# Performance work log

Measured on AMD Instinct MI355X. Metric: run time of the kernel, lower is better.

The kernel has to match this reference:

```python
import jax, jax.numpy as jnp
import numpy as np

D_MODEL = 1024
NUM_HEADS = 16
D_K = D_MODEL // NUM_HEADS
THETA = 10000.0


def setup_inputs() -> dict:
    key = jax.random.key(0)
    ks = jax.random.split(key, 5)
    b, s = 4, 1024
    std = 1.0 / np.sqrt(D_MODEL)
    x = jax.random.normal(ks[0], (b, s, D_MODEL), dtype=jnp.float32)
    token_positions = jnp.tile(jnp.arange(s, dtype=jnp.int64)[None, :], (b, 1))
    Wq = jax.random.truncated_normal(ks[1], -3.0, 3.0, (D_MODEL, D_MODEL), jnp.float32) * std
    Wk = jax.random.truncated_normal(ks[2], -3.0, 3.0, (D_MODEL, D_MODEL), jnp.float32) * std
    Wv = jax.random.truncated_normal(ks[3], -3.0, 3.0, (D_MODEL, D_MODEL), jnp.float32) * std
    Wo = jax.random.truncated_normal(ks[4], -3.0, 3.0, (D_MODEL, D_MODEL), jnp.float32) * std
    return {"x": x, "token_positions": token_positions,
            "Wq": Wq, "Wk": Wk, "Wv": Wv, "Wo": Wo}


def _apply_rope(x):
    # x: [b, h, s, d_k]; source uses row index i (ignores token_positions)
    s, d = x.shape[-2], x.shape[-1]
    pos = jnp.arange(s, dtype=jnp.float32)                      # [s]
    kidx = jnp.arange(0, d, 2, dtype=jnp.float32)               # [d/2]
    ang = pos[:, None] / (THETA ** (kidx / d))                  # [s, d/2]
    cos, sin = jnp.cos(ang), jnp.sin(ang)
    x_even, x_odd = x[..., 0::2], x[..., 1::2]                  # [b,h,s,d/2]
    out_even = x_even * cos - x_odd * sin
    out_odd = x_even * sin + x_odd * cos
    return jnp.stack([out_even, out_odd], axis=-1).reshape(x.shape)


def reference(x, token_positions, Wq, Wk, Wv, Wo):
    b, s, _ = x.shape
    # Linear: einsum '... din, dout din -> ... dout'  => x @ W.T
    q = jnp.einsum('bsd,ed->bse', x, Wq)
    k = jnp.einsum('bsd,ed->bse', x, Wk)
    v = jnp.einsum('bsd,ed->bse', x, Wv)
    # split heads -> [b, h, s, d_k]
    def split(t):
        return t.reshape(b, s, NUM_HEADS, D_K).transpose(0, 2, 1, 3)
    q, k, v = split(q), split(k), split(v)
    q = _apply_rope(q)
    k = _apply_rope(k)
    scores = jnp.einsum('bhqd,bhkd->bhqk', q, k) / np.sqrt(D_K)
    causal = jnp.tril(jnp.ones((s, s), dtype=bool))
    scores = jnp.where(causal, scores, -jnp.inf)
    attn = jax.nn.softmax(scores, axis=-1)
    out = jnp.einsum('bhqk,bhkd->bhqd', attn, v)
    out = out.transpose(0, 2, 1, 3).reshape(b, s, D_MODEL)
    return jnp.einsum('bsd,ed->bse', out, Wo)
```

## Files before the change

kernel.cpp:

```cpp
#include <hip/hip_runtime.h>

typedef __attribute__((ext_vector_type(8))) short short8;
typedef __attribute__((ext_vector_type(8))) __bf16 bf16x8;
typedef __attribute__((ext_vector_type(4))) float f32x4;
typedef __attribute__((ext_vector_type(4))) float float4v;
typedef __attribute__((ext_vector_type(2))) unsigned uint2v;
typedef __attribute__((ext_vector_type(4))) unsigned uint4v;

#define AS1 __attribute__((address_space(1)))
#define AS3 __attribute__((address_space(3)))

#define BATCH 4
#define SEQ 1024
#define DM 1024
#define NH 16
#define DKH 64
#define MROWS (BATCH * SEQ)
#define N3 (3 * DM)
#define LOG2E 1.4426950408889634f

static __device__ __forceinline__ unsigned short f2bf(float f) {
  unsigned u = __builtin_bit_cast(unsigned, f);
  u += 0x7FFFu + ((u >> 16) & 1u);
  return (unsigned short)(u >> 16);
}
static __device__ __forceinline__ float bf2f(unsigned short h) {
  return __builtin_bit_cast(float, ((unsigned)h) << 16);
}
static __device__ __forceinline__ unsigned cvt_pk_bf16(float lo, float hi) {
  unsigned r;
  asm("v_cvt_pk_bf16_f32 %0, %1, %2" : "=v"(r) : "v"(lo), "v"(hi));
  return r;
}
static __device__ __forceinline__ f32x4 mfma16(short8 a, short8 b, f32x4 c) {
  return __builtin_amdgcn_mfma_f32_16x16x32_bf16(
      __builtin_bit_cast(bf16x8, a), __builtin_bit_cast(bf16x8, b), c, 0, 0, 0);
}

__global__ __launch_bounds__(256) void convert_kernel(
    const float* __restrict__ x, const float* __restrict__ wq,
    const float* __restrict__ wk, const float* __restrict__ wv,
    const float* __restrict__ wo, unsigned short* __restrict__ xb,
    unsigned short* __restrict__ wqkv, unsigned short* __restrict__ wob) {
  size_t i4 = ((size_t)blockIdx.x * 256 + threadIdx.x) * 4;
  const size_t SZX = (size_t)MROWS * DM;
  const size_t SZW = (size_t)DM * DM;
  const float* src;
  unsigned short* dst;
  size_t off;
  if (i4 < SZX) {
    src = x; dst = xb; off = i4;
  } else if (i4 < SZX + SZW) {
    src = wq; dst = wqkv; off = i4 - SZX;
  } else if (i4 < SZX + 2 * SZW) {
    src = wk; dst = wqkv + SZW; off = i4 - SZX - SZW;
  } else if (i4 < SZX + 3 * SZW) {
    src = wv; dst = wqkv + 2 * SZW; off = i4 - SZX - 2 * SZW;
  } else {
    src = wo; dst = wob; off = i4 - SZX - 3 * SZW;
  }
  float4v v = *(const float4v*)(src + off);
  uint2v o;
  o.x = cvt_pk_bf16(v.x, v.y);
  o.y = cvt_pk_bf16(v.z, v.w);
  *(uint2v*)(dst + off) = o;
}

static __device__ __forceinline__ void store_c(float* p, float v) { *p = v; }
static __device__ __forceinline__ void store_c(unsigned short* p, float v) { *p = f2bf(v); }

template <typename OutT>
__global__ __launch_bounds__(256) void gemm_bt(
    const unsigned short* __restrict__ A, const unsigned short* __restrict__ B,
    OutT* __restrict__ C, int M, int N, int K) {
  __shared__ char sA[16384];
  __shared__ char sB[16384];
  const int tid = threadIdx.x, w = tid >> 6, lane = tid & 63;
  const int g = lane >> 4, r = lane & 15;
  const int m0 = blockIdx.y * 128, n0 = blockIdx.x * 128;
  const int wm = (w >> 1) * 64, wn = (w & 1) * 64;
  f32x4 acc[4][4] = {};
  for (int k0 = 0; k0 < K; k0 += 64) {
#pragma unroll
    for (int c = 0; c < 4; ++c) {
      int p = c * 4096 + tid * 16;
      int o = p ^ (((p >> 7) & 7) << 4);
      int row = o >> 7, colb = o & 127;
      const char* ga = (const char*)(A + (size_t)(m0 + row) * K + k0) + colb;
      const char* gb = (const char*)(B + (size_t)(n0 + row) * K + k0) + colb;
      __builtin_amdgcn_global_load_lds((const AS1 void*)ga,
                                       (AS3 void*)(sA + c * 4096 + (w << 10)), 16, 0, 0);
      __builtin_amdgcn_global_load_lds((const AS1 void*)gb,
                                       (AS3 void*)(sB + c * 4096 + (w << 10)), 16, 0, 0);
    }
    __syncthreads();
#pragma unroll
    for (int kk = 0; kk < 2; ++kk) {
      short8 af[4], bfr[4];
#pragma unroll
      for (int i = 0; i < 4; ++i) {
        int ra = wm + i * 16 + r;
        af[i] = *(const short8*)(sA + (((ra << 7) + (kk << 6) + (g << 4)) ^ ((ra & 7) << 4)));
        int rb = wn + i * 16 + r;
        bfr[i] = *(const short8*)(sB + (((rb << 7) + (kk << 6) + (g << 4)) ^ ((rb & 7) << 4)));
      }
#pragma unroll
      for (int i = 0; i < 4; ++i)
#pragma unroll
        for (int j = 0; j < 4; ++j) acc[i][j] = mfma16(af[i], bfr[j], acc[i][j]);
    }
    __syncthreads();
  }
#pragma unroll
  for (int i = 0; i < 4; ++i)
#pragma unroll
    for (int j = 0; j < 4; ++j)
#pragma unroll
      for (int jj = 0; jj < 4; ++jj) {
        int row = m0 + wm + i * 16 + g * 4 + jj;
        int col = n0 + wn + j * 16 + r;
        store_c(&C[(size_t)row * N + col], acc[i][j][jj]);
      }
}

__global__ __launch_bounds__(256) void gemm_n64(
    const unsigned short* __restrict__ A, const unsigned short* __restrict__ B,
    float* __restrict__ C, int M, int N, int K) {
  __shared__ char sA[16384];
  __shared__ char sB[8192];
  const int tid = threadIdx.x, w = tid >> 6, lane = tid & 63;
  const int g = lane >> 4, r = lane & 15;
  const int m0 = blockIdx.y * 128, n0 = blockIdx.x * 64;
  const int wm = (w >> 1) * 64, wn = (w & 1) * 32;
  f32x4 acc[4][2] = {};
  for (int k0 = 0; k0 < K; k0 += 64) {
#pragma unroll
    for (int c = 0; c < 4; ++c) {
      int p = c * 4096 + tid * 16;
      int o = p ^ (((p >> 7) & 7) << 4);
      int row = o >> 7, colb = o & 127;
      const char* ga = (const char*)(A + (size_t)(m0 + row) * K + k0) + colb;
      __builtin_amdgcn_global_load_lds((const AS1 void*)ga,
                                       (AS3 void*)(sA + c * 4096 + (w << 10)), 16, 0, 0);
      if (c < 2) {
        const char* gb = (const char*)(B + (size_t)(n0 + row) * K + k0) + colb;
        __builtin_amdgcn_global_load_lds((const AS1 void*)gb,
                                         (AS3 void*)(sB + c * 4096 + (w << 10)), 16, 0, 0);
      }
    }
    __syncthreads();
#pragma unroll
    for (int kk = 0; kk < 2; ++kk) {
      short8 af[4], bfr[2];
#pragma unroll
      for (int i = 0; i < 4; ++i) {
        int ra = wm + i * 16 + r;
        af[i] = *(const short8*)(sA + (((ra << 7) + (kk << 6) + (g << 4)) ^ ((ra & 7) << 4)));
      }
#pragma unroll
      for (int j = 0; j < 2; ++j) {
        int rb = wn + j * 16 + r;
        bfr[j] = *(const short8*)(sB + (((rb << 7) + (kk << 6) + (g << 4)) ^ ((rb & 7) << 4)));
      }
#pragma unroll
      for (int i = 0; i < 4; ++i)
#pragma unroll
        for (int j = 0; j < 2; ++j) acc[i][j] = mfma16(af[i], bfr[j], acc[i][j]);
    }
    __syncthreads();
  }
#pragma unroll
  for (int i = 0; i < 4; ++i)
#pragma unroll
    for (int j = 0; j < 2; ++j)
#pragma unroll
      for (int jj = 0; jj < 4; ++jj) {
        int row = m0 + wm + i * 16 + g * 4 + jj;
        int col = n0 + wn + j * 16 + r;
        C[(size_t)row * N + col] = acc[i][j][jj];
      }
}

__global__ __launch_bounds__(256) void rope_tv(const unsigned short* __restrict__ cf,
                                               unsigned short* __restrict__ qb,
                                               unsigned short* __restrict__ kb,
                                               unsigned short* __restrict__ vt) {
  __shared__ unsigned short tile[64][72];
  const int bid = blockIdx.x;
  if (bid < 2048) {
    int i = bid * 256 + threadIdx.x;
    int t8 = i & 7, h = (i >> 3) & 15, s = (i >> 7) & 1023, b = i >> 17;
    const unsigned short* src = cf + (size_t)(b * SEQ + s) * N3 + h * DKH + t8 * 8;
    short8 q8 = *(const short8*)src;
    short8 k8 = *(const short8*)(src + DM);
    uint4v qo, ko;
    const float qs = 0.125f * LOG2E;
#pragma unroll
    for (int p = 0; p < 4; ++p) {
      int kidx = t8 * 4 + p;
      float freq = __expf(-(float)kidx * 0.28782313662425572f);
      float sn, cs;
      __sincosf((float)s * freq, &sn, &cs);
      float qe = bf2f((unsigned short)q8[2 * p]), qv = bf2f((unsigned short)q8[2 * p + 1]);
      float ke = bf2f((unsigned short)k8[2 * p]), kv = bf2f((unsigned short)k8[2 * p + 1]);
      qo[p] = cvt_pk_bf16((qe * cs - qv * sn) * qs, (qe * sn + qv * cs) * qs);
      ko[p] = cvt_pk_bf16(ke * cs - kv * sn, ke * sn + kv * cs);
    }
    size_t dsto = (size_t)((b * NH + h) * SEQ + s) * DKH + t8 * 8;
    *(uint4v*)(qb + dsto) = qo;
    *(uint4v*)(kb + dsto) = ko;
  } else {
    int t = bid - 2048;
    int bh = t >> 4, b = bh >> 4, h = bh & 15, s0 = (t & 15) * 64;
    int tt = threadIdx.x, row = tt >> 2, c0 = (tt & 3) * 16;
    const unsigned short* src = cf + (size_t)(b * SEQ + s0 + row) * N3 + 2 * DM + h * DKH + c0;
    short8 v0 = *(const short8*)src;
    short8 v1 = *(const short8*)(src + 8);
    *(short8*)&tile[row][c0] = v0;
    *(short8*)&tile[row][c0 + 8] = v1;
    __syncthreads();
    unsigned short* dst = vt + ((size_t)bh * DKH + row) * SEQ + s0 + c0;
    short8 o0, o1;
#pragma unroll
    for (int j = 0; j < 8; ++j) o0[j] = (short)tile[c0 + j][row];
#pragma unroll
    for (int j = 0; j < 8; ++j) o1[j] = (short)tile[c0 + 8 + j][row];
    *(short8*)dst = o0;
    *(short8*)(dst + 8) = o1;
  }
}

__global__ __launch_bounds__(256) void attn_kernel(const unsigned short* __restrict__ qb,
                                                   const unsigned short* __restrict__ kb,
                                                   const unsigned short* __restrict__ vt,
                                                   unsigned short* __restrict__ ob) {
  __shared__ char kl[2][8192];
  __shared__ char vl[2][8192];
  __shared__ unsigned short plds[4][2][1024];
  const int bx = blockIdx.x, bh = blockIdx.y, b = bh >> 4, h = bh & 15;
  const int qlo = bx, qhi = 15 - bx;
  const int tid = threadIdx.x, w = tid >> 6, lane = tid & 63;
  const int g = lane >> 4, r = lane & 15;
  const float DEFER = 8.f * LOG2E;
  const unsigned short* Q = qb + (size_t)bh * SEQ * DKH;
  const char* Kp = (const char*)(kb + (size_t)bh * SEQ * DKH);
  const char* Vp = (const char*)(vt + (size_t)bh * DKH * SEQ);

  const int p0 = (w << 10) + lane * 16;
  const int p1 = p0 + 4096;
  const int o0 = p0 ^ (((p0 >> 7) & 7) << 4);
  const int o1 = p1 ^ (((p1 >> 7) & 7) << 4);
  const int r0 = o0 >> 7, c0 = o0 & 127, r1 = o1 >> 7, c1 = o1 & 127;
  const size_t ks0 = (size_t)r0 * 128 + c0, ks1 = (size_t)r1 * 128 + c1;
  const size_t vs0 = (size_t)r0 * 2048 + c0, vs1 = (size_t)r1 * 2048 + c1;

#define STAGE_KV(bi, kt)                                                          \
  do {                                                                            \
    const char* kbase = Kp + (size_t)(kt) * 8192;                                 \
    const char* vbase = Vp + (size_t)(kt) * 128;                                  \
    __builtin_amdgcn_global_load_lds((const AS1 void*)(kbase + ks0),              \
                                     (AS3 void*)(kl[bi] + p0), 16, 0, 0);         \
    __builtin_amdgcn_global_load_lds((const AS1 void*)(kbase + ks1),              \
                                     (AS3 void*)(kl[bi] + p1), 16, 0, 0);         \
    __builtin_amdgcn_global_load_lds((const AS1 void*)(vbase + vs0),              \
                                     (AS3 void*)(vl[bi] + p0), 16, 0, 0);         \
    __builtin_amdgcn_global_load_lds((const AS1 void*)(vbase + vs1),              \
                                     (AS3 void*)(vl[bi] + p1), 16, 0, 0);         \
  } while (0)

  short8 qfL0, qfL1, qfH0, qfH1;
  {
    int qrL = qlo * 64 + w * 16 + r;
    int qrH = qhi * 64 + w * 16 + r;
    qfL0 = *(const short8*)(Q + (size_t)qrL * DKH + g * 8);
    qfL1 = *(const short8*)(Q + (size_t)qrL * DKH + 32 + g * 8);
    qfH0 = *(const short8*)(Q + (size_t)qrH * DKH + g * 8);
    qfH1 = *(const short8*)(Q + (size_t)qrH * DKH + 32 + g * 8);
  }
  f32x4 oaccL[4] = {}, oaccH[4] = {};
  float mrunL = -1e30f, lrunL = 0.f, mrunH = -1e30f, lrunH = 0.f;
  const int qgH = qhi * 64 + w * 16 + r;
  const int qgL = qlo * 64 + w * 16 + r;
  char* pbH = (char*)&plds[w][0][0];
  char* pbL = (char*)&plds[w][1][0];

  STAGE_KV(0, 0);
  __syncthreads();

  for (int kt = 0; kt <= qhi; ++kt) {
    if (kt < qhi) STAGE_KV((kt + 1) & 1, kt + 1);
    const bool doLo = (kt <= qlo);
    const char* kb_ = kl[kt & 1];
    const char* vb_ = vl[kt & 1];
    f32x4 sh[4] = {}, sl[4] = {};
#pragma unroll
    for (int nb = 0; nb < 4; ++nb) {
      int ra = nb * 16 + r;
      short8 kf0 = *(const short8*)(kb_ + ((ra * 128 + g * 16) ^ ((ra & 7) << 4)));
      short8 kf1 = *(const short8*)(kb_ + ((ra * 128 + 64 + g * 16) ^ ((ra & 7) << 4)));
      sh[nb] = mfma16(kf0, qfH0, sh[nb]);
      sh[nb] = mfma16(kf1, qfH1, sh[nb]);
      if (doLo) {
        sl[nb] = mfma16(kf0, qfL0, sl[nb]);
        sl[nb] = mfma16(kf1, qfL1, sl[nb]);
      }
    }
    if (kt == qhi) {
#pragma unroll
      for (int nb = 0; nb < 4; ++nb)
#pragma unroll
        for (int j = 0; j < 4; ++j)
          if (kt * 64 + nb * 16 + g * 4 + j > qgH) sh[nb][j] = -1e30f;
    }
    if (kt == qlo) {
#pragma unroll
      for (int nb = 0; nb < 4; ++nb)
#pragma unroll
        for (int j = 0; j < 4; ++j)
          if (kt * 64 + nb * 16 + g * 4 + j > qgL) sl[nb][j] = -1e30f;
    }
    {
      float a0 = fmaxf(fmaxf(sh[0][0], sh[0][1]), fmaxf(sh[0][2], sh[0][3]));
      float a1 = fmaxf(fmaxf(sh[1][0], sh[1][1]), fmaxf(sh[1][2], sh[1][3]));
      float a2 = fmaxf(fmaxf(sh[2][0], sh[2][1]), fmaxf(sh[2][2], sh[2][3]));
      float a3 = fmaxf(fmaxf(sh[3][0], sh[3][1]), fmaxf(sh[3][2], sh[3][3]));
      float tm = fmaxf(fmaxf(a0, a1), fmaxf(a2, a3));
      tm = fmaxf(tm, __shfl_xor(tm, 16, 64));
      tm = fmaxf(tm, __shfl_xor(tm, 32, 64));
      if (!__all(tm <= mrunH + DEFER)) {
        float mnew = fmaxf(mrunH, tm);
        float scl = exp2f(mrunH - mnew);
        mrunH = mnew;
        lrunH *= scl;
#pragma unroll
        for (int db = 0; db < 4; ++db) {
          f32x4 t = oaccH[db];
          t[0] *= scl; t[1] *= scl; t[2] *= scl; t[3] *= scl;
          oaccH[db] = t;
        }
      }
      float ps = 0.f;
#pragma unroll
      for (int nb = 0; nb < 4; ++nb)
#pragma unroll
        for (int j = 0; j < 4; ++j) {
          float p = exp2f(sh[nb][j] - mrunH);
          sh[nb][j] = p;
          ps += p;
        }
      ps += __shfl_xor(ps, 16, 64);
      ps += __shfl_xor(ps, 32, 64);
      lrunH += ps;
#pragma unroll
      for (int nb = 0; nb < 4; ++nb) {
        uint2v pk;
        pk.x = cvt_pk_bf16(sh[nb][0], sh[nb][1]);
        pk.y = cvt_pk_bf16(sh[nb][2], sh[nb][3]);
        *(uint2v*)(pbH + ((r * 128 + nb * 32 + g * 8) ^ ((r & 7) << 4))) = pk;
      }
    }
    if (doLo) {
      float a0 = fmaxf(fmaxf(sl[0][0], sl[0][1]), fmaxf(sl[0][2], sl[0][3]));
      float a1 = fmaxf(fmaxf(sl[1][0], sl[1][1]), fmaxf(sl[1][2], sl[1][3]));
      float a2 = fmaxf(fmaxf(sl[2][0], sl[2][1]), fmaxf(sl[2][2], sl[2][3]));
      float a3 = fmaxf(fmaxf(sl[3][0], sl[3][1]), fmaxf(sl[3][2], sl[3][3]));
      float tm = fmaxf(fmaxf(a0, a1), fmaxf(a2, a3));
      tm = fmaxf(tm, __shfl_xor(tm, 16, 64));
      tm = fmaxf(tm, __shfl_xor(tm, 32, 64));
      if (!__all(tm <= mrunL + DEFER)) {
        float mnew = fmaxf(mrunL, tm);
        float scl = exp2f(mrunL - mnew);
        mrunL = mnew;
        lrunL *= scl;
#pragma unroll
        for (int db = 0; db < 4; ++db) {
          f32x4 t = oaccL[db];
          t[0] *= scl; t[1] *= scl; t[2] *= scl; t[3] *= scl;
          oaccL[db] = t;
        }
      }
      float ps = 0.f;
#pragma unroll
      for (int nb = 0; nb < 4; ++nb)
#pragma unroll
        for (int j = 0; j < 4; ++j) {
          float p = exp2f(sl[nb][j] - mrunL);
          sl[nb][j] = p;
          ps += p;
        }
      ps += __shfl_xor(ps, 16, 64);
      ps += __shfl_xor(ps, 32, 64);
      lrunL += ps;
#pragma unroll
      for (int nb = 0; nb < 4; ++nb) {
        uint2v pk;
        pk.x = cvt_pk_bf16(sl[nb][0], sl[nb][1]);
        pk.y = cvt_pk_bf16(sl[nb][2], sl[nb][3]);
        *(uint2v*)(pbL + ((r * 128 + nb * 32 + g * 8) ^ ((r & 7) << 4))) = pk;
      }
    }
    asm volatile("s_waitcnt lgkmcnt(0)" ::: "memory");
    __builtin_amdgcn_sched_barrier(0);
    short8 pfH0 = *(const short8*)(pbH + ((r * 128 + g * 16) ^ ((r & 7) << 4)));
    short8 pfH1 = *(const short8*)(pbH + ((r * 128 + 64 + g * 16) ^ ((r & 7) << 4)));
    short8 pfL0, pfL1;
    if (doLo) {
      pfL0 = *(const short8*)(pbL + ((r * 128 + g * 16) ^ ((r & 7) << 4)));
      pfL1 = *(const short8*)(pbL + ((r * 128 + 64 + g * 16) ^ ((r & 7) << 4)));
    }
#pragma unroll
    for (int db = 0; db < 4; ++db) {
      int rv = db * 16 + r;
      short8 vf0 = *(const short8*)(vb_ + ((rv * 128 + g * 16) ^ ((rv & 7) << 4)));
      short8 vf1 = *(const short8*)(vb_ + ((rv * 128 + 64 + g * 16) ^ ((rv & 7) << 4)));
      oaccH[db] = mfma16(vf0, pfH0, oaccH[db]);
      oaccH[db] = mfma16(vf1, pfH1, oaccH[db]);
      if (doLo) {
        oaccL[db] = mfma16(vf0, pfL0, oaccL[db]);
        oaccL[db] = mfma16(vf1, pfL1, oaccL[db]);
      }
    }
    __syncthreads();
  }
  {
    float invH = 1.f / lrunH;
    unsigned short* orH = ob + (size_t)(b * SEQ + qgH) * DM + h * DKH;
#pragma unroll
    for (int db = 0; db < 4; ++db) {
      uint2v pk;
      pk.x = cvt_pk_bf16(oaccH[db][0] * invH, oaccH[db][1] * invH);
      pk.y = cvt_pk_bf16(oaccH[db][2] * invH, oaccH[db][3] * invH);
      *(uint2v*)(orH + db * 16 + g * 4) = pk;
    }
    float invL = 1.f / lrunL;
    unsigned short* orL = ob + (size_t)(b * SEQ + qgL) * DM + h * DKH;
#pragma unroll
    for (int db = 0; db < 4; ++db) {
      uint2v pk;
      pk.x = cvt_pk_bf16(oaccL[db][0] * invL, oaccL[db][1] * invL);
      pk.y = cvt_pk_bf16(oaccL[db][2] * invL, oaccL[db][3] * invL);
      *(uint2v*)(orL + db * 16 + g * 4) = pk;
    }
  }
#undef STAGE_KV
}

extern "C" void kernel_launch(void* const* d_in, const int* in_sizes, int n_in,
                              void* d_out, int out_size, void* d_ws, size_t ws_size,
                              hipStream_t stream) {
  const float* x = (const float*)d_in[0];
  const float* wq = (const float*)d_in[2];
  const float* wk = (const float*)d_in[3];
  const float* wv = (const float*)d_in[4];
  const float* wo = (const float*)d_in[5];
  char* ws = (char*)d_ws;
  unsigned short* xb = (unsigned short*)(ws);
  unsigned short* wqkv = (unsigned short*)(ws + (8u << 20));
  unsigned short* wob = (unsigned short*)(ws + (14u << 20));
  unsigned short* cf = (unsigned short*)(ws + (16u << 20));
  unsigned short* qbuf = (unsigned short*)(ws + (40u << 20));
  unsigned short* kbuf = (unsigned short*)(ws + (48u << 20));
  unsigned short* vtb = (unsigned short*)(ws + (56u << 20));
  unsigned short* obuf = (unsigned short*)(ws + (64u << 20));
  float* out = (float*)d_out;

  convert_kernel<<<8192, 256, 0, stream>>>(x, wq, wk, wv, wo, xb, wqkv, wob);
  gemm_bt<unsigned short><<<dim3(24, 32), 256, 0, stream>>>(xb, wqkv, cf, MROWS, N3, DM);
  rope_tv<<<3072, 256, 0, stream>>>(cf, qbuf, kbuf, vtb);
  attn_kernel<<<dim3(8, 64), 256, 0, stream>>>(qbuf, kbuf, vtb, obuf);
  gemm_n64<<<dim3(16, 32), 256, 0, stream>>>(obuf, wob, out, MROWS, DM, DM);
}
```

Before: 108.3 us.

## Replace paired causal query blocks with one query block per workgroup

The attention kernel no longer pairs a low and a high query tile in each workgroup to balance causal work. Each block now handles one 64-row query tile, and the grid doubles to 16x64, with the heaviest tiles scheduled first. This halves per-block registers and LDS for P, which may raise occupancy and parallelism. In exchange, K/V tiles shared by the pair are now loaded twice, and block durations become uneven.

```diff
diff --git a/kernel.cpp b/kernel.cpp
--- a/kernel.cpp
+++ b/kernel.cpp
@@ -236,9 +236,9 @@
                                                    unsigned short* __restrict__ ob) {
   __shared__ char kl[2][8192];
   __shared__ char vl[2][8192];
-  __shared__ unsigned short plds[4][2][1024];
+  __shared__ unsigned short plds[4][1024];
   const int bx = blockIdx.x, bh = blockIdx.y, b = bh >> 4, h = bh & 15;
-  const int qlo = bx, qhi = 15 - bx;
+  const int qblk = 15 - bx;
   const int tid = threadIdx.x, w = tid >> 6, lane = tid & 63;
   const int g = lane >> 4, r = lane & 15;
   const float DEFER = 8.f * LOG2E;
@@ -268,56 +268,39 @@
                                      (AS3 void*)(vl[bi] + p1), 16, 0, 0);         \
   } while (0)
 
-  short8 qfL0, qfL1, qfH0, qfH1;
+  short8 qf0, qf1;
   {
-    int qrL = qlo * 64 + w * 16 + r;
-    int qrH = qhi * 64 + w * 16 + r;
-    qfL0 = *(const short8*)(Q + (size_t)qrL * DKH + g * 8);
-    qfL1 = *(const short8*)(Q + (size_t)qrL * DKH + 32 + g * 8);
-    qfH0 = *(const short8*)(Q + (size_t)qrH * DKH + g * 8);
-    qfH1 = *(const short8*)(Q + (size_t)qrH * DKH + 32 + g * 8);
-  }
-  f32x4 oaccL[4] = {}, oaccH[4] = {};
-  float mrunL = -1e30f, lrunL = 0.f, mrunH = -1e30f, lrunH = 0.f;
-  const int qgH = qhi * 64 + w * 16 + r;
-  const int qgL = qlo * 64 + w * 16 + r;
-  char* pbH = (char*)&plds[w][0][0];
-  char* pbL = (char*)&plds[w][1][0];
+    int qrow = qblk * 64 + w * 16 + r;
+    qf0 = *(const short8*)(Q + (size_t)qrow * DKH + g * 8);
+    qf1 = *(const short8*)(Q + (size_t)qrow * DKH + 32 + g * 8);
+  }
+  f32x4 oacc[4] = {};
+  float mrun = -1e30f, lrun = 0.f;
+  const int qg = qblk * 64 + w * 16 + r;
+  char* pbase = (char*)&plds[w][0];
 
   STAGE_KV(0, 0);
   __syncthreads();
 
-  for (int kt = 0; kt <= qhi; ++kt) {
-    if (kt < qhi) STAGE_KV((kt + 1) & 1, kt + 1);
-    const bool doLo = (kt <= qlo);
+  for (int kt = 0; kt <= qblk; ++kt) {
+    if (kt < qblk) STAGE_KV((kt + 1) & 1, kt + 1);
     const char* kb_ = kl[kt & 1];
     const char* vb_ = vl[kt & 1];
-    f32x4 sh[4] = {}, sl[4] = {};
+    f32x4 sh[4] = {};
 #pragma unroll
     for (int nb = 0; nb < 4; ++nb) {
       int ra = nb * 16 + r;
       short8 kf0 = *(const short8*)(kb_ + ((ra * 128 + g * 16) ^ ((ra & 7) << 4)));
       short8 kf1 = *(const short8*)(kb_ + ((ra * 128 + 64 + g * 16) ^ ((ra & 7) << 4)));
-      sh[nb] = mfma16(kf0, qfH0, sh[nb]);
-      sh[nb] = mfma16(kf1, qfH1, sh[nb]);
-      if (doLo) {
-        sl[nb] = mfma16(kf0, qfL0, sl[nb]);
-        sl[nb] = mfma16(kf1, qfL1, sl[nb]);
-      }
-    }
-    if (kt == qhi) {
+      sh[nb] = mfma16(kf0, qf0, sh[nb]);
+      sh[nb] = mfma16(kf1, qf1, sh[nb]);
+    }
+    if (kt == qblk) {
 #pragma unroll
       for (int nb = 0; nb < 4; ++nb)
 #pragma unroll
         for (int j = 0; j < 4; ++j)
-          if (kt * 64 + nb * 16 + g * 4 + j > qgH) sh[nb][j] = -1e30f;
-    }
-    if (kt == qlo) {
-#pragma unroll
-      for (int nb = 0; nb < 4; ++nb)
-#pragma unroll
-        for (int j = 0; j < 4; ++j)
-          if (kt * 64 + nb * 16 + g * 4 + j > qgL) sl[nb][j] = -1e30f;
+          if (kt * 64 + nb * 16 + g * 4 + j > qg) sh[nb][j] = -1e30f;
     }
     {
       float a0 = fmaxf(fmaxf(sh[0][0], sh[0][1]), fmaxf(sh[0][2], sh[0][3]));
@@ -327,16 +310,16 @@
       float tm = fmaxf(fmaxf(a0, a1), fmaxf(a2, a3));
       tm = fmaxf(tm, __shfl_xor(tm, 16, 64));
       tm = fmaxf(tm, __shfl_xor(tm, 32, 64));
-      if (!__all(tm <= mrunH + DEFER)) {
-        float mnew = fmaxf(mrunH, tm);
-        float scl = exp2f(mrunH - mnew);
-        mrunH = mnew;
-        lrunH *= scl;
+      if (!__all(tm <= mrun + DEFER)) {
+        float mnew = fmaxf(mrun, tm);
+        float scl = exp2f(mrun - mnew);
+        mrun = mnew;
+        lrun *= scl;
 #pragma unroll
         for (int db = 0; db < 4; ++db) {
-          f32x4 t = oaccH[db];
+          f32x4 t = oacc[db];
           t[0] *= scl; t[1] *= scl; t[2] *= scl; t[3] *= scl;
-          oaccH[db] = t;
+          oacc[db] = t;
         }
       }
       float ps = 0.f;
@@ -344,102 +327,44 @@
       for (int nb = 0; nb < 4; ++nb)
 #pragma unroll
         for (int j = 0; j < 4; ++j) {
-          float p = exp2f(sh[nb][j] - mrunH);
+          float p = exp2f(sh[nb][j] - mrun);
           sh[nb][j] = p;
           ps += p;
         }
       ps += __shfl_xor(ps, 16, 64);
       ps += __shfl_xor(ps, 32, 64);
-      lrunH += ps;
+      lrun += ps;
 #pragma unroll
       for (int nb = 0; nb < 4; ++nb) {
         uint2v pk;
         pk.x = cvt_pk_bf16(sh[nb][0], sh[nb][1]);
         pk.y = cvt_pk_bf16(sh[nb][2], sh[nb][3]);
-        *(uint2v*)(pbH + ((r * 128 + nb * 32 + g * 8) ^ ((r & 7) << 4))) = pk;
-      }
-    }
-    if (doLo) {
-      float a0 = fmaxf(fmaxf(sl[0][0], sl[0][1]), fmaxf(sl[0][2], sl[0][3]));
-      float a1 = fmaxf(fmaxf(sl[1][0], sl[1][1]), fmaxf(sl[1][2], sl[1][3]));
-      float a2 = fmaxf(fmaxf(sl[2][0], sl[2][1]), fmaxf(sl[2][2], sl[2][3]));
-      float a3 = fmaxf(fmaxf(sl[3][0], sl[3][1]), fmaxf(sl[3][2], sl[3][3]));
-      float tm = fmaxf(fmaxf(a0, a1), fmaxf(a2, a3));
-      tm = fmaxf(tm, __shfl_xor(tm, 16, 64));
-      tm = fmaxf(tm, __shfl_xor(tm, 32, 64));
-      if (!__all(tm <= mrunL + DEFER)) {
-        float mnew = fmaxf(mrunL, tm);
-        float scl = exp2f(mrunL - mnew);
-        mrunL = mnew;
-        lrunL *= scl;
-#pragma unroll
-        for (int db = 0; db < 4; ++db) {
-          f32x4 t = oaccL[db];
-          t[0] *= scl; t[1] *= scl; t[2] *= scl; t[3] *= scl;
-          oaccL[db] = t;
-        }
-      }
-      float ps = 0.f;
-#pragma unroll
-      for (int nb = 0; nb < 4; ++nb)
-#pragma unroll
-        for (int j = 0; j < 4; ++j) {
-          float p = exp2f(sl[nb][j] - mrunL);
-          sl[nb][j] = p;
-          ps += p;
-        }
-      ps += __shfl_xor(ps, 16, 64);
-      ps += __shfl_xor(ps, 32, 64);
-      lrunL += ps;
-#pragma unroll
-      for (int nb = 0; nb < 4; ++nb) {
-        uint2v pk;
-        pk.x = cvt_pk_bf16(sl[nb][0], sl[nb][1]);
-        pk.y = cvt_pk_bf16(sl[nb][2], sl[nb][3]);
-        *(uint2v*)(pbL + ((r * 128 + nb * 32 + g * 8) ^ ((r & 7) << 4))) = pk;
+        *(uint2v*)(pbase + ((r * 128 + nb * 32 + g * 8) ^ ((r & 7) << 4))) = pk;
       }
     }
     asm volatile("s_waitcnt lgkmcnt(0)" ::: "memory");
     __builtin_amdgcn_sched_barrier(0);
-    short8 pfH0 = *(const short8*)(pbH + ((r * 128 + g * 16) ^ ((r & 7) << 4)));
-    short8 pfH1 = *(const short8*)(pbH + ((r * 128 + 64 + g * 16) ^ ((r & 7) << 4)));
-    short8 pfL0, pfL1;
-    if (doLo) {
-      pfL0 = *(const short8*)(pbL + ((r * 128 + g * 16) ^ ((r & 7) << 4)));
-      pfL1 = *(const short8*)(pbL + ((r * 128 + 64 + g * 16) ^ ((r & 7) << 4)));
-    }
+    short8 pf0 = *(const short8*)(pbase + ((r * 128 + g * 16) ^ ((r & 7) << 4)));
+    short8 pf1 = *(const short8*)(pbase + ((r * 128 + 64 + g * 16) ^ ((r & 7) << 4)));
 #pragma unroll
     for (int db = 0; db < 4; ++db) {
       int rv = db * 16 + r;
       short8 vf0 = *(const short8*)(vb_ + ((rv * 128 + g * 16) ^ ((rv & 7) << 4)));
       short8 vf1 = *(const short8*)(vb_ + ((rv * 128 + 64 + g * 16) ^ ((rv & 7) << 4)));
-      oaccH[db] = mfma16(vf0, pfH0, oaccH[db]);
-      oaccH[db] = mfma16(vf1, pfH1, oaccH[db]);
-      if (doLo) {
-        oaccL[db] = mfma16(vf0, pfL0, oaccL[db]);
-        oaccL[db] = mfma16(vf1, pfL1, oaccL[db]);
-      }
+      oacc[db] = mfma16(vf0, pf0, oacc[db]);
+      oacc[db] = mfma16(vf1, pf1, oacc[db]);
     }
     __syncthreads();
   }
   {
-    float invH = 1.f / lrunH;
-    unsigned short* orH = ob + (size_t)(b * SEQ + qgH) * DM + h * DKH;
+    float inv = 1.f / lrun;
+    unsigned short* orow = ob + (size_t)(b * SEQ + qg) * DM + h * DKH;
 #pragma unroll
     for (int db = 0; db < 4; ++db) {
       uint2v pk;
-      pk.x = cvt_pk_bf16(oaccH[db][0] * invH, oaccH[db][1] * invH);
-      pk.y = cvt_pk_bf16(oaccH[db][2] * invH, oaccH[db][3] * invH);
-      *(uint2v*)(orH + db * 16 + g * 4) = pk;
-    }
-    float invL = 1.f / lrunL;
-    unsigned short* orL = ob + (size_t)(b * SEQ + qgL) * DM + h * DKH;
-#pragma unroll
-    for (int db = 0; db < 4; ++db) {
-      uint2v pk;
-      pk.x = cvt_pk_bf16(oaccL[db][0] * invL, oaccL[db][1] * invL);
-      pk.y = cvt_pk_bf16(oaccL[db][2] * invL, oaccL[db][3] * invL);
-      *(uint2v*)(orL + db * 16 + g * 4) = pk;
+      pk.x = cvt_pk_bf16(oacc[db][0] * inv, oacc[db][1] * inv);
+      pk.y = cvt_pk_bf16(oacc[db][2] * inv, oacc[db][3] * inv);
+      *(uint2v*)(orow + db * 16 + g * 4) = pk;
     }
   }
 #undef STAGE_KV
@@ -467,6 +392,6 @@
   convert_kernel<<<8192, 256, 0, stream>>>(x, wq, wk, wv, wo, xb, wqkv, wob);
   gemm_bt<unsigned short><<<dim3(24, 32), 256, 0, stream>>>(xb, wqkv, cf, MROWS, N3, DM);
   rope_tv<<<3072, 256, 0, stream>>>(cf, qbuf, kbuf, vtb);
-  attn_kernel<<<dim3(8, 64), 256, 0, stream>>>(qbuf, kbuf, vtb, obuf);
+  attn_kernel<<<dim3(16, 64), 256, 0, stream>>>(qbuf, kbuf, vtb, obuf);
   gemm_n64<<<dim3(16, 32), 256, 0, stream>>>(obuf, wob, out, MROWS, DM, DM);
 }
```

Measured after the change: 114.7 us. +5.9%, slower.
